# Kernel optimization log

Measured on AMD Instinct MI355X. Metric: run time of the kernel, lower is better.

## Reference

```python
import jax, jax.numpy as jnp
import numpy as np

EPS = 1e-5  # BatchNorm eps

def gcn_conv(x, src, dst, deg, dinv, W, b):
    # PyG GCNConv: out = D^{-1/2}(A+I)D^{-1/2} X W + b
    N = x.shape[0]
    xw = x @ W                               # [N, F_out]
    norm = dinv[src] * dinv[dst]             # [E]
    agg = jax.ops.segment_sum(xw[src] * norm[:, None], dst, num_segments=N)
    agg = agg + xw * (1.0 / deg)[:, None]    # self-loop term: deg^-1/2 * deg^-1/2
    return agg + b

def bn(x, g, b, m, v):
    # inference-mode BatchNorm1d over features
    return (x - m) * jax.lax.rsqrt(v + EPS) * g + b

def setup_inputs() -> dict:
    key = jax.random.key(0)
    N, E, F_in, C = 100000, 1600000, 128, 16
    dims = [F_in, 64, 128, 64, 32, C]
    ks = jax.random.split(key, 64)
    inp = {}
    inp["x"] = jax.random.normal(ks[0], (N, F_in), dtype=jnp.float32)
    inp["edge_index"] = jax.random.randint(ks[1], (2, E), 0, N, dtype=jnp.int32)
    ki = 2
    for l in range(5):
        fi, fo = dims[l], dims[l + 1]
        scale = 1.0 / np.sqrt(fi)
        inp[f"w{l+1}"] = jax.random.normal(ks[ki], (fi, fo), dtype=jnp.float32) * scale; ki += 1
        inp[f"b{l+1}"] = jnp.zeros((fo,), dtype=jnp.float32)
    for l in range(4):  # BN params for layers 1..4
        fo = dims[l + 1]
        inp[f"g{l+1}"] = jnp.ones((fo,), dtype=jnp.float32)
        inp[f"be{l+1}"] = jnp.zeros((fo,), dtype=jnp.float32)
        inp[f"m{l+1}"] = jax.random.normal(ks[ki], (fo,), dtype=jnp.float32) * 0.1; ki += 1
        inp[f"v{l+1}"] = jax.random.uniform(ks[ki], (fo,), dtype=jnp.float32, minval=0.5, maxval=1.5); ki += 1
    return inp

def reference(x, edge_index,
              w1, b1, w2, b2, w3, b3, w4, b4, w5, b5,
              g1, be1, m1, v1, g2, be2, m2, v2,
              g3, be3, m3, v3, g4, be4, m4, v4):
    N = x.shape[0]
    src, dst = edge_index[0], edge_index[1]
    deg = jax.ops.segment_sum(jnp.ones(src.shape[0], x.dtype), dst, num_segments=N) + 1.0
    dinv = jax.lax.rsqrt(deg)
    h = jax.nn.relu(bn(gcn_conv(x, src, dst, deg, dinv, w1, b1), g1, be1, m1, v1))
    h = jax.nn.relu(bn(gcn_conv(h, src, dst, deg, dinv, w2, b2), g2, be2, m2, v2))
    h = jax.nn.relu(bn(gcn_conv(h, src, dst, deg, dinv, w3, b3), g3, be3, m3, v3))
    h = jax.nn.relu(bn(gcn_conv(h, src, dst, deg, dinv, w4, b4), g4, be4, m4, v4))
    return gcn_conv(h, src, dst, deg, dinv, w5, b5)
```

## Files before the change

kernel.cpp:

```cpp
#include <hip/hip_runtime.h>
#include <hip/hip_fp16.h>

#define BEPS 1e-5f
static constexpr int TPB = 256;
static constexpr int G_SC = 512;
static constexpr int BK_SHIFT = 8;
static constexpr int BK_NODES = 256;
static constexpr int KMAX = 512;
static constexpr int BK_SLACK = 2048;

union F4H8 { float4 f4; __half2 h2[4]; };

typedef _Float16 half8 __attribute__((ext_vector_type(8)));
typedef float floatx4 __attribute__((ext_vector_type(4)));


__global__ __launch_bounds__(TPB) void k_zero_int(int* __restrict__ p, int n) {
  int i = blockIdx.x * TPB + threadIdx.x;
  if (i < n) p[i] = 0;
}

__global__ __launch_bounds__(TPB) void k_hist(const int* __restrict__ dst,
                                              int* __restrict__ histG,
                                              int* __restrict__ btot,
                                              int E, int K, int chunk) {
  __shared__ int lh[KMAX];
  int g = blockIdx.x, t = threadIdx.x;
  for (int i = t; i < KMAX; i += TPB) lh[i] = 0;
  __syncthreads();
  int e0 = g * chunk, e1 = min(E, e0 + chunk);
  for (int e = e0 + t; e < e1; e += TPB) atomicAdd(&lh[dst[e] >> BK_SHIFT], 1);
  __syncthreads();
  for (int i = t; i < K; i += TPB) {
    histG[i * G_SC + g] = lh[i];
    atomicAdd(&btot[i], lh[i]);
  }
}

__global__ __launch_bounds__(KMAX) void k_bbase(const int* __restrict__ btot,
                                                int* __restrict__ bbase, int K) {
  __shared__ int sh[KMAX];
  int t = threadIdx.x;
  int v = (t < K) ? btot[t] : 0;
  sh[t] = v;
  __syncthreads();
  for (int s = 1; s < KMAX; s <<= 1) {
    int x = sh[t];
    int y = (t >= s) ? sh[t - s] : 0;
    __syncthreads();
    sh[t] = x + y;
    __syncthreads();
  }
  if (t < K) bbase[t] = sh[t] - v;
  if (t == 0) bbase[K] = sh[K - 1];
}

__global__ __launch_bounds__(G_SC) void k_offs(const int* __restrict__ histG,
                                               const int* __restrict__ bbase,
                                               int* __restrict__ offs) {
  __shared__ int sh[G_SC];
  int b = blockIdx.x, t = threadIdx.x;
  int v = histG[b * G_SC + t];
  sh[t] = v;
  __syncthreads();
  for (int s = 1; s < G_SC; s <<= 1) {
    int x = sh[t];
    int y = (t >= s) ? sh[t - s] : 0;
    __syncthreads();
    sh[t] = x + y;
    __syncthreads();
  }
  offs[b * G_SC + t] = bbase[b] + sh[t] - v;
}

__global__ __launch_bounds__(TPB) void k_scatter(const int* __restrict__ src,
                                                 const int* __restrict__ dst,
                                                 const int* __restrict__ offs,
                                                 unsigned int* __restrict__ pairs,
                                                 int E, int K, int chunk) {
  __shared__ int cur[KMAX];
  int g = blockIdx.x, t = threadIdx.x;
  for (int i = t; i < K; i += TPB) cur[i] = offs[i * G_SC + g];
  __syncthreads();
  int e0 = g * chunk, e1 = min(E, e0 + chunk);
  for (int e = e0 + t; e < e1; e += TPB) {
    int d = dst[e];
    int b = d >> BK_SHIFT;
    int pos = atomicAdd(&cur[b], 1);
    pairs[pos] = (unsigned int)src[e] | ((unsigned int)(d & (BK_NODES - 1)) << 20);
  }
}

__global__ __launch_bounds__(TPB) void k_bucket_sort(const unsigned int* __restrict__ pairs,
                                                     const int* __restrict__ bbase,
                                                     int* __restrict__ rowptr,
                                                     int* __restrict__ rowend,
                                                     int* __restrict__ colidx,
                                                     float* __restrict__ dinv,
                                                     int N, int E) {
  __shared__ int cur[BK_NODES];
  __shared__ int sh[BK_NODES];
  int b = blockIdx.x, t = threadIdx.x;
  int base = bbase[b], end = bbase[b + 1];
  int n0 = b << BK_SHIFT;
  int nNodes = min(BK_NODES, N - n0);
  cur[t] = 0;
  __syncthreads();
  for (int e = base + t; e < end; e += TPB) atomicAdd(&cur[pairs[e] >> 20], 1);
  __syncthreads();
  int v = cur[t];
  int pd = (v + 7) & ~7;
  sh[t] = pd;
  __syncthreads();
  for (int s = 1; s < TPB; s <<= 1) {
    int x = sh[t];
    int y = (t >= s) ? sh[t - s] : 0;
    __syncthreads();
    sh[t] = x + y;
    __syncthreads();
  }
  int Bb = (base + b * BK_SLACK + 7) & ~7;
  int start = Bb + (sh[t] - pd);
  if (t < nNodes) {
    rowptr[n0 + t] = start;
    rowend[n0 + t] = start + pd;
    dinv[n0 + t] = rsqrtf((float)(v + 1));
    for (int i = start + v; i < start + pd; ++i) colidx[i] = N;
  }
  __syncthreads();
  cur[t] = start;
  __syncthreads();
  for (int e = base + t; e < end; e += TPB) {
    unsigned int p = pairs[e];
    int pos = atomicAdd(&cur[p >> 20], 1);
    colidx[pos] = (int)(p & 0xFFFFFu);
  }
}

__device__ inline void packone(const float* __restrict__ W, _Float16* __restrict__ Wp,
                               int i, int FO) {
  int j = i & 7, lane = (i >> 3) & 63, tile = i >> 9;
  int nct = FO >> 4, ct = tile % nct, kch = tile / nct;
  int k = kch * 32 + ((lane >> 4) << 3) + j;
  int n = (ct << 4) + (lane & 15);
  Wp[i] = (_Float16)W[k * FO + n];
}

__global__ __launch_bounds__(TPB) void k_packAll(const float* w1, _Float16* p1,
                                                 const float* w2, _Float16* p2,
                                                 const float* w3, _Float16* p3,
                                                 const float* w4, _Float16* p4,
                                                 const float* w5, _Float16* p5,
                                                 __half* bufA, int N) {
  int i = blockIdx.x * TPB + threadIdx.x;
  if (i < 8192) packone(w1, p1, i, 64);
  else if (i < 16384) packone(w2, p2, i - 8192, 128);
  else if (i < 24576) packone(w3, p3, i - 16384, 64);
  else if (i < 26624) packone(w4, p4, i - 24576, 32);
  else if (i < 27136) packone(w5, p5, i - 26624, 16);
  else if (i < 27144) {
    float4 z = {0.f, 0.f, 0.f, 0.f};
    reinterpret_cast<float4*>(bufA + (size_t)64 * N)[i - 27136] = z;
  }
}

template <int FI, int FO, int EPI, bool F32IN>
__global__ __launch_bounds__(TPB) void k_mgemm(const void* __restrict__ hin,
                                               const _Float16* __restrict__ Wp,
                                               const float* __restrict__ dinv,
                                               const float* __restrict__ bias,
                                               const float* __restrict__ g,
                                               const float* __restrict__ be,
                                               const float* __restrict__ m,
                                               const float* __restrict__ v,
                                               __half* __restrict__ out, int N) {
  constexpr int NCT = FO / 16;
  constexpr int NKC = FI / 32;
  __shared__ float4 Wsh[NKC * NCT * 64];
  for (int i = threadIdx.x; i < NKC * NCT * 64; i += TPB)
    Wsh[i] = reinterpret_cast<const float4*>(Wp)[i];
  __syncthreads();

  int lane = threadIdx.x & 63;
  int wv = threadIdx.x >> 6;
  int quad = lane >> 4;
  int rowBase = blockIdx.x * 64 + wv * 16;
  int rA = min(rowBase + (lane & 15), N - 1);

  floatx4 acc[NCT];
#pragma unroll
  for (int ct = 0; ct < NCT; ++ct) acc[ct] = (floatx4){0.f, 0.f, 0.f, 0.f};

#pragma unroll
  for (int kch = 0; kch < NKC; ++kch) {
    half8 a;
    if constexpr (F32IN) {
      const float4* xp = reinterpret_cast<const float4*>(hin);
      size_t idx = ((size_t)rA * FI + kch * 32 + quad * 8) >> 2;
      float4 fa = xp[idx], fb = xp[idx + 1];
      a[0] = (_Float16)fa.x; a[1] = (_Float16)fa.y; a[2] = (_Float16)fa.z; a[3] = (_Float16)fa.w;
      a[4] = (_Float16)fb.x; a[5] = (_Float16)fb.y; a[6] = (_Float16)fb.z; a[7] = (_Float16)fb.w;
    } else {
      union { float4 f4; half8 h8; } ua;
      ua.f4 = reinterpret_cast<const float4*>(hin)[((size_t)rA * FI + kch * 32 + quad * 8) >> 3];
      a = ua.h8;
    }
#pragma unroll
    for (int ct = 0; ct < NCT; ++ct) {
      union { float4 f4; half8 h8; } ub;
      ub.f4 = Wsh[(kch * NCT + ct) * 64 + lane];
      acc[ct] = __builtin_amdgcn_mfma_f32_16x16x32_f16(a, ub.h8, acc[ct], 0, 0, 0);
    }
  }

  int r0 = rowBase + quad * 4;
  if (EPI == 0) {
    float dv[4];
#pragma unroll
    for (int reg = 0; reg < 4; ++reg) dv[reg] = (r0 + reg < N) ? dinv[r0 + reg] : 0.f;
#pragma unroll
    for (int ct = 0; ct < NCT; ++ct) {
      int col = ct * 16 + (lane & 15);
#pragma unroll
      for (int reg = 0; reg < 4; ++reg) {
        int r = r0 + reg;
        out[(size_t)r * FO + col] = __float2half(acc[ct][reg] * dv[reg]);
      }
    }
  } else {
#pragma unroll
    for (int ct = 0; ct < NCT; ++ct) {
      int col = ct * 16 + (lane & 15);
      float sc = g[col] * rsqrtf(v[col] + BEPS);
      float bb = bias[col] - m[col];
      float ee = be[col];
#pragma unroll
      for (int reg = 0; reg < 4; ++reg) {
        int r = r0 + reg;
        out[(size_t)r * FO + col] = __float2half(fmaxf((acc[ct][reg] + bb) * sc + ee, 0.f));
      }
    }
  }
}

__global__ __launch_bounds__(TPB) void k_mgemm23(const __half* __restrict__ hin,
                                                 const _Float16* __restrict__ W2p,
                                                 const _Float16* __restrict__ W3p,
                                                 const float* __restrict__ dinv,
                                                 const float* __restrict__ b2,
                                                 const float* __restrict__ g2,
                                                 const float* __restrict__ be2,
                                                 const float* __restrict__ m2,
                                                 const float* __restrict__ v2,
                                                 __half* __restrict__ out, int N) {
  __shared__ float4 W2s[2 * 8 * 64];
  __shared__ float4 W3s[4 * 4 * 64];
  __shared__ _Float16 tr[4 * 16 * 136];
  for (int i = threadIdx.x; i < 1024; i += TPB) W2s[i] = reinterpret_cast<const float4*>(W2p)[i];
  for (int i = threadIdx.x; i < 1024; i += TPB) W3s[i] = reinterpret_cast<const float4*>(W3p)[i];
  __syncthreads();

  int lane = threadIdx.x & 63;
  int wv = threadIdx.x >> 6;
  int quad = lane >> 4;
  int m = lane & 15;
  int rowBase = blockIdx.x * 64 + wv * 16;
  int rA = min(rowBase + m, N - 1);

  floatx4 acc1[8];
#pragma unroll
  for (int ct = 0; ct < 8; ++ct) acc1[ct] = (floatx4){0.f, 0.f, 0.f, 0.f};
#pragma unroll
  for (int kch = 0; kch < 2; ++kch) {
    union { float4 f4; half8 h8; } ua;
    ua.f4 = reinterpret_cast<const float4*>(hin)[((size_t)rA * 64 + kch * 32 + quad * 8) >> 3];
#pragma unroll
    for (int ct = 0; ct < 8; ++ct) {
      union { float4 f4; half8 h8; } ub;
      ub.f4 = W2s[(kch * 8 + ct) * 64 + lane];
      acc1[ct] = __builtin_amdgcn_mfma_f32_16x16x32_f16(ua.h8, ub.h8, acc1[ct], 0, 0, 0);
    }
  }
  _Float16* mytr = tr + wv * 16 * 136;
#pragma unroll
  for (int ct = 0; ct < 8; ++ct) {
    int col = ct * 16 + m;
    float sc = g2[col] * rsqrtf(v2[col] + BEPS);
    float bb = b2[col] - m2[col];
    float ee = be2[col];
#pragma unroll
    for (int reg = 0; reg < 4; ++reg) {
      int r = quad * 4 + reg;
      mytr[r * 136 + col] = (_Float16)fmaxf((acc1[ct][reg] + bb) * sc + ee, 0.f);
    }
  }
  floatx4 acc2[4];
#pragma unroll
  for (int ct = 0; ct < 4; ++ct) acc2[ct] = (floatx4){0.f, 0.f, 0.f, 0.f};
#pragma unroll
  for (int kch = 0; kch < 4; ++kch) {
    half8 a2 = *reinterpret_cast<const half8*>(&mytr[m * 136 + kch * 32 + quad * 8]);
#pragma unroll
    for (int ct = 0; ct < 4; ++ct) {
      union { float4 f4; half8 h8; } ub;
      ub.f4 = W3s[(kch * 4 + ct) * 64 + lane];
      acc2[ct] = __builtin_amdgcn_mfma_f32_16x16x32_f16(a2, ub.h8, acc2[ct], 0, 0, 0);
    }
  }
  int r0 = rowBase + quad * 4;
  float dv[4];
#pragma unroll
  for (int reg = 0; reg < 4; ++reg) dv[reg] = (r0 + reg < N) ? dinv[r0 + reg] : 0.f;
#pragma unroll
  for (int ct = 0; ct < 4; ++ct) {
    int col = ct * 16 + m;
#pragma unroll
    for (int reg = 0; reg < 4; ++reg) {
      int r = r0 + reg;
      out[(size_t)r * 64 + col] = __float2half(acc2[ct][reg] * dv[reg]);
    }
  }
}

template <int F, int MODE, typename TO>
__global__ __launch_bounds__(TPB) void k_agg(const __half* __restrict__ in,
                                             const int* __restrict__ rowptr,
                                             const int* __restrict__ rowend,
                                             const int* __restrict__ colidx,
                                             const float* __restrict__ dinv,
                                             const float* __restrict__ bias,
                                             const float* __restrict__ g,
                                             const float* __restrict__ be,
                                             const float* __restrict__ m,
                                             const float* __restrict__ v,
                                             TO* __restrict__ out, int N) {
  constexpr int V = F / 8;
  constexpr int NPB = TPB / V;
  int node = blockIdx.x * NPB + (int)(threadIdx.x / V);
  int lane = threadIdx.x % V;
  if (node >= N) return;
  const float4* in16 = reinterpret_cast<const float4*>(in);
  const size_t rs = F / 8;
  float acc[8];
  {
    F4H8 u;
    u.f4 = in16[(size_t)node * rs + lane];
#pragma unroll
    for (int i = 0; i < 4; ++i) {
      float2 t2 = __half22float2(u.h2[i]);
      acc[2 * i] = t2.x;
      acc[2 * i + 1] = t2.y;
    }
  }
  int e0 = rowptr[node], e1 = rowend[node];
  int e = e0;
  for (; e + 16 <= e1; e += 16) {
    int4 c0 = *reinterpret_cast<const int4*>(colidx + e);
    int4 c1 = *reinterpret_cast<const int4*>(colidx + e + 4);
    int4 c2 = *reinterpret_cast<const int4*>(colidx + e + 8);
    int4 c3 = *reinterpret_cast<const int4*>(colidx + e + 12);
    F4H8 u[16];
    u[0].f4  = in16[(size_t)c0.x * rs + lane];
    u[1].f4  = in16[(size_t)c0.y * rs + lane];
    u[2].f4  = in16[(size_t)c0.z * rs + lane];
    u[3].f4  = in16[(size_t)c0.w * rs + lane];
    u[4].f4  = in16[(size_t)c1.x * rs + lane];
    u[5].f4  = in16[(size_t)c1.y * rs + lane];
    u[6].f4  = in16[(size_t)c1.z * rs + lane];
    u[7].f4  = in16[(size_t)c1.w * rs + lane];
    u[8].f4  = in16[(size_t)c2.x * rs + lane];
    u[9].f4  = in16[(size_t)c2.y * rs + lane];
    u[10].f4 = in16[(size_t)c2.z * rs + lane];
    u[11].f4 = in16[(size_t)c2.w * rs + lane];
    u[12].f4 = in16[(size_t)c3.x * rs + lane];
    u[13].f4 = in16[(size_t)c3.y * rs + lane];
    u[14].f4 = in16[(size_t)c3.z * rs + lane];
    u[15].f4 = in16[(size_t)c3.w * rs + lane];
#pragma unroll
    for (int q = 0; q < 16; ++q) {
#pragma unroll
      for (int i = 0; i < 4; ++i) {
        float2 t2 = __half22float2(u[q].h2[i]);
        acc[2 * i] += t2.x;
        acc[2 * i + 1] += t2.y;
      }
    }
  }
  if (e < e1) {
    int4 c0 = *reinterpret_cast<const int4*>(colidx + e);
    int4 c1 = *reinterpret_cast<const int4*>(colidx + e + 4);
    F4H8 u[8];
    u[0].f4 = in16[(size_t)c0.x * rs + lane];
    u[1].f4 = in16[(size_t)c0.y * rs + lane];
    u[2].f4 = in16[(size_t)c0.z * rs + lane];
    u[3].f4 = in16[(size_t)c0.w * rs + lane];
    u[4].f4 = in16[(size_t)c1.x * rs + lane];
    u[5].f4 = in16[(size_t)c1.y * rs + lane];
    u[6].f4 = in16[(size_t)c1.z * rs + lane];
    u[7].f4 = in16[(size_t)c1.w * rs + lane];
#pragma unroll
    for (int q = 0; q < 8; ++q) {
#pragma unroll
      for (int i = 0; i < 4; ++i) {
        float2 t2 = __half22float2(u[q].h2[i]);
        acc[2 * i] += t2.x;
        acc[2 * i + 1] += t2.y;
      }
    }
  }
  float dv = dinv[node];
#pragma unroll
  for (int i = 0; i < 8; ++i) acc[i] *= dv;
  if (MODE == 0) {
    float4 ba = reinterpret_cast<const float4*>(bias)[lane * 2];
    float4 bb = reinterpret_cast<const float4*>(bias)[lane * 2 + 1];
    acc[0] += ba.x; acc[1] += ba.y; acc[2] += ba.z; acc[3] += ba.w;
    acc[4] += bb.x; acc[5] += bb.y; acc[6] += bb.z; acc[7] += bb.w;
  } else if (MODE == 1 || MODE == 2) {
    const float4* B = reinterpret_cast<const float4*>(bias);
    const float4* G = reinterpret_cast<const float4*>(g);
    const float4* Be = reinterpret_cast<const float4*>(be);
    const float4* M = reinterpret_cast<const float4*>(m);
    const float4* Vv = reinterpret_cast<const float4*>(v);
#pragma unroll
    for (int h = 0; h < 2; ++h) {
      float4 b4 = B[lane * 2 + h], g4 = G[lane * 2 + h], e4 = Be[lane * 2 + h];
      float4 m4 = M[lane * 2 + h], v4 = Vv[lane * 2 + h];
      float* a = acc + 4 * h;
      a[0] = fmaxf((a[0] + b4.x - m4.x) * (g4.x * rsqrtf(v4.x + BEPS)) + e4.x, 0.f);
      a[1] = fmaxf((a[1] + b4.y - m4.y) * (g4.y * rsqrtf(v4.y + BEPS)) + e4.y, 0.f);
      a[2] = fmaxf((a[2] + b4.z - m4.z) * (g4.z * rsqrtf(v4.z + BEPS)) + e4.z, 0.f);
      a[3] = fmaxf((a[3] + b4.w - m4.w) * (g4.w * rsqrtf(v4.w + BEPS)) + e4.w, 0.f);
    }
    if (MODE == 2) {
#pragma unroll
      for (int i = 0; i < 8; ++i) acc[i] *= dv;
    }
  }
  if constexpr (sizeof(TO) == 2) {
    F4H8 u;
#pragma unroll
    for (int i = 0; i < 4; ++i) u.h2[i] = __floats2half2_rn(acc[2 * i], acc[2 * i + 1]);
    reinterpret_cast<float4*>(out)[(size_t)node * rs + lane] = u.f4;
  } else {
    float4 o0 = {acc[0], acc[1], acc[2], acc[3]};
    float4 o1 = {acc[4], acc[5], acc[6], acc[7]};
    float4* op = reinterpret_cast<float4*>((float*)out + (size_t)node * F + lane * 8);
    op[0] = o0;
    op[1] = o1;
  }
}


extern "C" void kernel_launch(void* const* d_in, const int* in_sizes, int n_in,
                              void* d_out, int out_size, void* d_ws, size_t ws_size,
                              hipStream_t stream) {
  const float* x = (const float*)d_in[0];
  const int* ei = (const int*)d_in[1];
  const int N = in_sizes[0] / 128;
  const int E = in_sizes[1] / 2;
  const int* src = ei;
  const int* dst = ei + E;

  const float* w1 = (const float*)d_in[2];  const float* b1 = (const float*)d_in[3];
  const float* w2 = (const float*)d_in[4];  const float* b2 = (const float*)d_in[5];
  const float* w3 = (const float*)d_in[6];  const float* b3 = (const float*)d_in[7];
  const float* w4 = (const float*)d_in[8];  const float* b4 = (const float*)d_in[9];
  const float* w5 = (const float*)d_in[10]; const float* b5 = (const float*)d_in[11];
  const float* g1 = (const float*)d_in[12]; const float* be1 = (const float*)d_in[13];
  const float* m1 = (const float*)d_in[14]; const float* v1 = (const float*)d_in[15];
  const float* g2 = (const float*)d_in[16]; const float* be2 = (const float*)d_in[17];
  const float* m2 = (const float*)d_in[18]; const float* v2 = (const float*)d_in[19];
  const float* g3 = (const float*)d_in[20]; const float* be3 = (const float*)d_in[21];
  const float* m3 = (const float*)d_in[22]; const float* v3 = (const float*)d_in[23];
  const float* g4 = (const float*)d_in[24]; const float* be4 = (const float*)d_in[25];
  const float* m4 = (const float*)d_in[26]; const float* v4 = (const float*)d_in[27];
  float* out = (float*)d_out;

  char* ws = (char*)d_ws;
  size_t off = 0;
  auto alloc = [&](size_t bytes) -> void* {
    void* p = ws + off;
    off += (bytes + 255) & ~(size_t)255;
    return p;
  };
  const int K = (N + BK_NODES - 1) >> BK_SHIFT;
  float*        dinv   = (float*)alloc((size_t)N * 4);
  int*          rowptr = (int*)alloc((size_t)N * 4);
  int*          rowend = (int*)alloc((size_t)N * 4);
  int*          colidx = (int*)alloc(((size_t)E + (size_t)(K + 1) * BK_SLACK) * 4);
  unsigned int* pairs  = (unsigned int*)alloc((size_t)E * 4);
  int*          histG  = (int*)alloc((size_t)KMAX * G_SC * 4);
  int*          offs   = (int*)alloc((size_t)KMAX * G_SC * 4);
  int*          btot   = (int*)alloc(KMAX * 4);
  int*          bbase  = (int*)alloc((KMAX + 1) * 4);
  _Float16*     wp1    = (_Float16*)alloc(128 * 64 * 2);
  _Float16*     wp2    = (_Float16*)alloc(64 * 128 * 2);
  _Float16*     wp3    = (_Float16*)alloc(128 * 64 * 2);
  _Float16*     wp4    = (_Float16*)alloc(64 * 32 * 2);
  _Float16*     wp5    = (_Float16*)alloc(32 * 16 * 2);
  __half*       bufA   = (__half*)alloc((size_t)(N + 64) * 128 * 2);
  __half*       bufB   = (__half*)alloc((size_t)(N + 64) * 128 * 2);
  (void)ws_size; (void)n_in; (void)out_size;

  const int chunk = (E + G_SC - 1) / G_SC;

  k_zero_int<<<2, TPB, 0, stream>>>(btot, KMAX);
  k_hist<<<G_SC, TPB, 0, stream>>>(dst, histG, btot, E, K, chunk);
  k_bbase<<<1, KMAX, 0, stream>>>(btot, bbase, K);
  k_offs<<<K, G_SC, 0, stream>>>(histG, bbase, offs);
  k_scatter<<<G_SC, TPB, 0, stream>>>(src, dst, offs, pairs, E, K, chunk);
  k_bucket_sort<<<K, TPB, 0, stream>>>(pairs, bbase, rowptr, rowend, colidx, dinv, N, E);

  k_packAll<<<(27144 + TPB - 1) / TPB, TPB, 0, stream>>>(w1, wp1, w2, wp2, w3, wp3, w4, wp4, w5, wp5, bufA, N);

  int gRow = (N + 63) / 64;
  k_mgemm<128, 64, 0, true><<<gRow, TPB, 0, stream>>>(x, wp1, dinv, nullptr, nullptr, nullptr, nullptr, nullptr, bufB, N);
  k_agg<64, 2, __half><<<(N + 31) / 32, TPB, 0, stream>>>(bufB, rowptr, rowend, colidx, dinv, b1, g1, be1, m1, v1, bufA, N);
  k_agg<64, 3, __half><<<(N + 31) / 32, TPB, 0, stream>>>(bufA, rowptr, rowend, colidx, dinv, nullptr, nullptr, nullptr, nullptr, nullptr, bufB, N);
  k_mgemm23<<<gRow, TPB, 0, stream>>>(bufB, wp2, wp3, dinv, b2, g2, be2, m2, v2, bufA, N);
  k_agg<64, 1, __half><<<(N + 31) / 32, TPB, 0, stream>>>(bufA, rowptr, rowend, colidx, dinv, b3, g3, be3, m3, v3, bufB, N);
  k_mgemm<64, 32, 0, false><<<gRow, TPB, 0, stream>>>(bufB, wp4, dinv, nullptr, nullptr, nullptr, nullptr, nullptr, bufA, N);
  k_agg<32, 1, __half><<<(N + 63) / 64, TPB, 0, stream>>>(bufA, rowptr, rowend, colidx, dinv, b4, g4, be4, m4, v4, bufB, N);
  k_mgemm<32, 16, 0, false><<<gRow, TPB, 0, stream>>>(bufB, wp5, dinv, nullptr, nullptr, nullptr, nullptr, nullptr, bufA, N);
  k_agg<16, 0, float><<<(N + 127) / 128, TPB, 0, stream>>>(bufA, rowptr, rowend, colidx, dinv, b5, nullptr, nullptr, nullptr, nullptr, out, N);
}
```

Before: 360.4 us.

## Fuse neighbor aggregation into following GEMM kernels for layers two through five

Replaces the separate aggregate-then-GEMM kernel pairs for the later layers with fused kernels that gather neighbor rows, apply normalization and BN/ReLU in registers, and feed the result straight into MFMA. This removes intermediate feature-buffer writes and reads and several launches. The histogram and scatter preprocessing kernels also switch to int4 vectorized edge loads, with the chunk size rounded up to a multiple of four. The fused gather assigns one node per 16-lane group with 4-way unrolling, so it may have less memory-level parallelism than the dedicated aggregation kernel. It also relies on column lists being padded to multiples of four.

```diff
diff --git a/kernel.cpp b/kernel.cpp
--- a/kernel.cpp
+++ b/kernel.cpp
@@ -29,7 +29,17 @@
   for (int i = t; i < KMAX; i += TPB) lh[i] = 0;
   __syncthreads();
   int e0 = g * chunk, e1 = min(E, e0 + chunk);
-  for (int e = e0 + t; e < e1; e += TPB) atomicAdd(&lh[dst[e] >> BK_SHIFT], 1);
+  for (int e = e0 + t * 4; e < e1; e += TPB * 4) {
+    if (e + 4 <= e1) {
+      int4 d4 = *reinterpret_cast<const int4*>(dst + e);
+      atomicAdd(&lh[d4.x >> BK_SHIFT], 1);
+      atomicAdd(&lh[d4.y >> BK_SHIFT], 1);
+      atomicAdd(&lh[d4.z >> BK_SHIFT], 1);
+      atomicAdd(&lh[d4.w >> BK_SHIFT], 1);
+    } else {
+      for (int q = e; q < e1; ++q) atomicAdd(&lh[dst[q] >> BK_SHIFT], 1);
+    }
+  }
   __syncthreads();
   for (int i = t; i < K; i += TPB) {
     histG[i * G_SC + g] = lh[i];
@@ -83,11 +93,25 @@
   for (int i = t; i < K; i += TPB) cur[i] = offs[i * G_SC + g];
   __syncthreads();
   int e0 = g * chunk, e1 = min(E, e0 + chunk);
-  for (int e = e0 + t; e < e1; e += TPB) {
-    int d = dst[e];
-    int b = d >> BK_SHIFT;
-    int pos = atomicAdd(&cur[b], 1);
-    pairs[pos] = (unsigned int)src[e] | ((unsigned int)(d & (BK_NODES - 1)) << 20);
+  for (int e = e0 + t * 4; e < e1; e += TPB * 4) {
+    if (e + 4 <= e1) {
+      int4 d4 = *reinterpret_cast<const int4*>(dst + e);
+      int4 s4 = *reinterpret_cast<const int4*>(src + e);
+      int p0 = atomicAdd(&cur[d4.x >> BK_SHIFT], 1);
+      pairs[p0] = (unsigned int)s4.x | ((unsigned int)(d4.x & (BK_NODES - 1)) << 20);
+      int p1 = atomicAdd(&cur[d4.y >> BK_SHIFT], 1);
+      pairs[p1] = (unsigned int)s4.y | ((unsigned int)(d4.y & (BK_NODES - 1)) << 20);
+      int p2 = atomicAdd(&cur[d4.z >> BK_SHIFT], 1);
+      pairs[p2] = (unsigned int)s4.z | ((unsigned int)(d4.z & (BK_NODES - 1)) << 20);
+      int p3 = atomicAdd(&cur[d4.w >> BK_SHIFT], 1);
+      pairs[p3] = (unsigned int)s4.w | ((unsigned int)(d4.w & (BK_NODES - 1)) << 20);
+    } else {
+      for (int q = e; q < e1; ++q) {
+        int d = dst[q];
+        int pos = atomicAdd(&cur[d >> BK_SHIFT], 1);
+        pairs[pos] = (unsigned int)src[q] | ((unsigned int)(d & (BK_NODES - 1)) << 20);
+      }
+    }
   }
 }
 
@@ -214,45 +238,98 @@
   }
 
   int r0 = rowBase + quad * 4;
-  if (EPI == 0) {
-    float dv[4];
-#pragma unroll
-    for (int reg = 0; reg < 4; ++reg) dv[reg] = (r0 + reg < N) ? dinv[r0 + reg] : 0.f;
-#pragma unroll
-    for (int ct = 0; ct < NCT; ++ct) {
-      int col = ct * 16 + (lane & 15);
-#pragma unroll
-      for (int reg = 0; reg < 4; ++reg) {
-        int r = r0 + reg;
-        out[(size_t)r * FO + col] = __float2half(acc[ct][reg] * dv[reg]);
+  float dv[4];
+#pragma unroll
+  for (int reg = 0; reg < 4; ++reg) dv[reg] = (r0 + reg < N) ? dinv[r0 + reg] : 0.f;
+#pragma unroll
+  for (int ct = 0; ct < NCT; ++ct) {
+    int col = ct * 16 + (lane & 15);
+#pragma unroll
+    for (int reg = 0; reg < 4; ++reg) {
+      int r = r0 + reg;
+      out[(size_t)r * FO + col] = __float2half(acc[ct][reg] * dv[reg]);
+    }
+  }
+  (void)bias; (void)g; (void)be; (void)m; (void)v;
+}
+
+template <int DO_BN>
+__device__ inline void agg_gather64(const float4* __restrict__ in16,
+                                    const int* __restrict__ rowptr,
+                                    const int* __restrict__ rowend,
+                                    const int* __restrict__ colidx,
+                                    const float* __restrict__ dinv,
+                                    const float* __restrict__ b_,
+                                    const float* __restrict__ g_,
+                                    const float* __restrict__ be_,
+                                    const float* __restrict__ m_,
+                                    const float* __restrict__ v_,
+                                    int node, int quad, int N, half8 afr[2]) {
+  bool valid = node < N;
+  int rd = valid ? node : N;
+  int e0 = valid ? rowptr[node] : 0;
+  int e1 = valid ? rowend[node] : 0;
+  float acc[2][8];
+#pragma unroll
+  for (int kch = 0; kch < 2; ++kch) {
+    F4H8 u;
+    u.f4 = in16[(size_t)rd * 8 + kch * 4 + quad];
+#pragma unroll
+    for (int i = 0; i < 4; ++i) {
+      float2 t2 = __half22float2(u.h2[i]);
+      acc[kch][2 * i] = t2.x;
+      acc[kch][2 * i + 1] = t2.y;
+    }
+  }
+  for (int e = e0; e < e1; e += 4) {
+    int4 c = *reinterpret_cast<const int4*>(colidx + e);
+#pragma unroll
+    for (int kch = 0; kch < 2; ++kch) {
+      int g = kch * 4 + quad;
+      F4H8 u0, u1, u2, u3;
+      u0.f4 = in16[(size_t)c.x * 8 + g];
+      u1.f4 = in16[(size_t)c.y * 8 + g];
+      u2.f4 = in16[(size_t)c.z * 8 + g];
+      u3.f4 = in16[(size_t)c.w * 8 + g];
+#pragma unroll
+      for (int i = 0; i < 4; ++i) {
+        float2 a = __half22float2(u0.h2[i]), b = __half22float2(u1.h2[i]);
+        float2 cc = __half22float2(u2.h2[i]), d = __half22float2(u3.h2[i]);
+        acc[kch][2 * i] += (a.x + b.x) + (cc.x + d.x);
+        acc[kch][2 * i + 1] += (a.y + b.y) + (cc.y + d.y);
       }
     }
-  } else {
-#pragma unroll
-    for (int ct = 0; ct < NCT; ++ct) {
-      int col = ct * 16 + (lane & 15);
-      float sc = g[col] * rsqrtf(v[col] + BEPS);
-      float bb = bias[col] - m[col];
-      float ee = be[col];
-#pragma unroll
-      for (int reg = 0; reg < 4; ++reg) {
-        int r = r0 + reg;
-        out[(size_t)r * FO + col] = __float2half(fmaxf((acc[ct][reg] + bb) * sc + ee, 0.f));
+  }
+  float dv = valid ? dinv[node] : 0.f;
+#pragma unroll
+  for (int kch = 0; kch < 2; ++kch) {
+    int f0 = kch * 32 + quad * 8;
+#pragma unroll
+    for (int j = 0; j < 8; ++j) {
+      float val = acc[kch][j] * dv;
+      if (DO_BN) {
+        int f = f0 + j;
+        float sc = g_[f] * rsqrtf(v_[f] + BEPS);
+        val = fmaxf((val + b_[f] - m_[f]) * sc + be_[f], 0.f);
       }
-    }
-  }
-}
-
-__global__ __launch_bounds__(TPB) void k_mgemm23(const __half* __restrict__ hin,
-                                                 const _Float16* __restrict__ W2p,
-                                                 const _Float16* __restrict__ W3p,
-                                                 const float* __restrict__ dinv,
-                                                 const float* __restrict__ b2,
-                                                 const float* __restrict__ g2,
-                                                 const float* __restrict__ be2,
-                                                 const float* __restrict__ m2,
-                                                 const float* __restrict__ v2,
-                                                 __half* __restrict__ out, int N) {
+      afr[kch][j] = (_Float16)val;
+    }
+  }
+}
+
+__global__ __launch_bounds__(TPB) void k_aggemm23(const __half* __restrict__ hin,
+                                                  const int* __restrict__ rowptr,
+                                                  const int* __restrict__ rowend,
+                                                  const int* __restrict__ colidx,
+                                                  const _Float16* __restrict__ W2p,
+                                                  const _Float16* __restrict__ W3p,
+                                                  const float* __restrict__ dinv,
+                                                  const float* __restrict__ b2,
+                                                  const float* __restrict__ g2,
+                                                  const float* __restrict__ be2,
+                                                  const float* __restrict__ m2,
+                                                  const float* __restrict__ v2,
+                                                  __half* __restrict__ out, int N) {
   __shared__ float4 W2s[2 * 8 * 64];
   __shared__ float4 W3s[4 * 4 * 64];
   __shared__ _Float16 tr[4 * 16 * 136];
@@ -265,20 +342,21 @@
   int quad = lane >> 4;
   int m = lane & 15;
   int rowBase = blockIdx.x * 64 + wv * 16;
-  int rA = min(rowBase + m, N - 1);
+
+  half8 afr[2];
+  agg_gather64<0>(reinterpret_cast<const float4*>(hin), rowptr, rowend, colidx, dinv,
+                  nullptr, nullptr, nullptr, nullptr, nullptr, rowBase + m, quad, N, afr);
 
   floatx4 acc1[8];
 #pragma unroll
   for (int ct = 0; ct < 8; ++ct) acc1[ct] = (floatx4){0.f, 0.f, 0.f, 0.f};
 #pragma unroll
   for (int kch = 0; kch < 2; ++kch) {
-    union { float4 f4; half8 h8; } ua;
-    ua.f4 = reinterpret_cast<const float4*>(hin)[((size_t)rA * 64 + kch * 32 + quad * 8) >> 3];
 #pragma unroll
     for (int ct = 0; ct < 8; ++ct) {
       union { float4 f4; half8 h8; } ub;
       ub.f4 = W2s[(kch * 8 + ct) * 64 + lane];
-      acc1[ct] = __builtin_amdgcn_mfma_f32_16x16x32_f16(ua.h8, ub.h8, acc1[ct], 0, 0, 0);
+      acc1[ct] = __builtin_amdgcn_mfma_f32_16x16x32_f16(afr[kch], ub.h8, acc1[ct], 0, 0, 0);
     }
   }
   _Float16* mytr = tr + wv * 16 * 136;
@@ -319,6 +397,138 @@
       int r = r0 + reg;
       out[(size_t)r * 64 + col] = __float2half(acc2[ct][reg] * dv[reg]);
     }
+  }
+}
+
+template <int FO>
+__global__ __launch_bounds__(TPB) void k_aggemm64(const __half* __restrict__ hin,
+                                                  const int* __restrict__ rowptr,
+                                                  const int* __restrict__ rowend,
+                                                  const int* __restrict__ colidx,
+                                                  const _Float16* __restrict__ Wp,
+                                                  const float* __restrict__ dinv,
+                                                  const float* __restrict__ b_,
+                                                  const float* __restrict__ g_,
+                                                  const float* __restrict__ be_,
+                                                  const float* __restrict__ m_,
+                                                  const float* __restrict__ v_,
+                                                  __half* __restrict__ out, int N) {
+  constexpr int NCT = FO / 16;
+  __shared__ float4 Wsh[2 * NCT * 64];
+  for (int i = threadIdx.x; i < 2 * NCT * 64; i += TPB)
+    Wsh[i] = reinterpret_cast<const float4*>(Wp)[i];
+  __syncthreads();
+
+  int lane = threadIdx.x & 63;
+  int wv = threadIdx.x >> 6;
+  int quad = lane >> 4;
+  int m = lane & 15;
+  int rowBase = blockIdx.x * 64 + wv * 16;
+
+  half8 afr[2];
+  agg_gather64<1>(reinterpret_cast<const float4*>(hin), rowptr, rowend, colidx, dinv,
+                  b_, g_, be_, m_, v_, rowBase + m, quad, N, afr);
+
+  floatx4 acc[NCT];
+#pragma unroll
+  for (int ct = 0; ct < NCT; ++ct) acc[ct] = (floatx4){0.f, 0.f, 0.f, 0.f};
+#pragma unroll
+  for (int kch = 0; kch < 2; ++kch) {
+#pragma unroll
+    for (int ct = 0; ct < NCT; ++ct) {
+      union { float4 f4; half8 h8; } ub;
+      ub.f4 = Wsh[(kch * NCT + ct) * 64 + lane];
+      acc[ct] = __builtin_amdgcn_mfma_f32_16x16x32_f16(afr[kch], ub.h8, acc[ct], 0, 0, 0);
+    }
+  }
+  int r0 = rowBase + quad * 4;
+  float dv[4];
+#pragma unroll
+  for (int reg = 0; reg < 4; ++reg) dv[reg] = (r0 + reg < N) ? dinv[r0 + reg] : 0.f;
+#pragma unroll
+  for (int ct = 0; ct < NCT; ++ct) {
+    int col = ct * 16 + m;
+#pragma unroll
+    for (int reg = 0; reg < 4; ++reg) {
+      int r = r0 + reg;
+      out[(size_t)r * FO + col] = __float2half(acc[ct][reg] * dv[reg]);
+    }
+  }
+}
+
+__global__ __launch_bounds__(TPB) void k_aggemm5(const __half* __restrict__ hin,
+                                                 const int* __restrict__ rowptr,
+                                                 const int* __restrict__ rowend,
+                                                 const int* __restrict__ colidx,
+                                                 const _Float16* __restrict__ Wp,
+                                                 const float* __restrict__ dinv,
+                                                 const float* __restrict__ b_,
+                                                 const float* __restrict__ g_,
+                                                 const float* __restrict__ be_,
+                                                 const float* __restrict__ m_,
+                                                 const float* __restrict__ v_,
+                                                 __half* __restrict__ out, int N) {
+  __shared__ float4 Wsh[64];
+  if (threadIdx.x < 64) Wsh[threadIdx.x] = reinterpret_cast<const float4*>(Wp)[threadIdx.x];
+  __syncthreads();
+
+  int lane = threadIdx.x & 63;
+  int wv = threadIdx.x >> 6;
+  int quad = lane >> 4;
+  int m = lane & 15;
+  int rowBase = blockIdx.x * 64 + wv * 16;
+  int node = rowBase + m;
+  bool valid = node < N;
+  int rd = valid ? node : N;
+  int e0 = valid ? rowptr[node] : 0;
+  int e1 = valid ? rowend[node] : 0;
+  const float4* in16 = reinterpret_cast<const float4*>(hin);
+
+  float acc[8];
+  {
+    F4H8 u;
+    u.f4 = in16[(size_t)rd * 4 + quad];
+#pragma unroll
+    for (int i = 0; i < 4; ++i) {
+      float2 t2 = __half22float2(u.h2[i]);
+      acc[2 * i] = t2.x;
+      acc[2 * i + 1] = t2.y;
+    }
+  }
+  for (int e = e0; e < e1; e += 4) {
+    int4 c = *reinterpret_cast<const int4*>(colidx + e);
+    F4H8 u0, u1, u2, u3;
+    u0.f4 = in16[(size_t)c.x * 4 + quad];
+    u1.f4 = in16[(size_t)c.y * 4 + quad];
+    u2.f4 = in16[(size_t)c.z * 4 + quad];
+    u3.f4 = in16[(size_t)c.w * 4 + quad];
+#pragma unroll
+    for (int i = 0; i < 4; ++i) {
+      float2 a = __half22float2(u0.h2[i]), b = __half22float2(u1.h2[i]);
+      float2 cc = __half22float2(u2.h2[i]), d = __half22float2(u3.h2[i]);
+      acc[2 * i] += (a.x + b.x) + (cc.x + d.x);
+      acc[2 * i + 1] += (a.y + b.y) + (cc.y + d.y);
+    }
+  }
+  float dvn = valid ? dinv[node] : 0.f;
+  half8 afr;
+#pragma unroll
+  for (int j = 0; j < 8; ++j) {
+    int f = quad * 8 + j;
+    float sc = g_[f] * rsqrtf(v_[f] + BEPS);
+    float val = fmaxf((acc[j] * dvn + b_[f] - m_[f]) * sc + be_[f], 0.f);
+    afr[j] = (_Float16)val;
+  }
+  floatx4 c0 = (floatx4){0.f, 0.f, 0.f, 0.f};
+  union { float4 f4; half8 h8; } ub;
+  ub.f4 = Wsh[lane];
+  c0 = __builtin_amdgcn_mfma_f32_16x16x32_f16(afr, ub.h8, c0, 0, 0, 0);
+  int r0 = rowBase + quad * 4;
+#pragma unroll
+  for (int reg = 0; reg < 4; ++reg) {
+    int r = r0 + reg;
+    float dv = (r < N) ? dinv[r] : 0.f;
+    out[(size_t)r * 16 + m] = __float2half(c0[reg] * dv);
   }
 }
 
@@ -354,39 +564,7 @@
   }
   int e0 = rowptr[node], e1 = rowend[node];
   int e = e0;
-  for (; e + 16 <= e1; e += 16) {
-    int4 c0 = *reinterpret_cast<const int4*>(colidx + e);
-    int4 c1 = *reinterpret_cast<const int4*>(colidx + e + 4);
-    int4 c2 = *reinterpret_cast<const int4*>(colidx + e + 8);
-    int4 c3 = *reinterpret_cast<const int4*>(colidx + e + 12);
-    F4H8 u[16];
-    u[0].f4  = in16[(size_t)c0.x * rs + lane];
-    u[1].f4  = in16[(size_t)c0.y * rs + lane];
-    u[2].f4  = in16[(size_t)c0.z * rs + lane];
-    u[3].f4  = in16[(size_t)c0.w * rs + lane];
-    u[4].f4  = in16[(size_t)c1.x * rs + lane];
-    u[5].f4  = in16[(size_t)c1.y * rs + lane];
-    u[6].f4  = in16[(size_t)c1.z * rs + lane];
-    u[7].f4  = in16[(size_t)c1.w * rs + lane];
-    u[8].f4  = in16[(size_t)c2.x * rs + lane];
-    u[9].f4  = in16[(size_t)c2.y * rs + lane];
-    u[10].f4 = in16[(size_t)c2.z * rs + lane];
-    u[11].f4 = in16[(size_t)c2.w * rs + lane];
-    u[12].f4 = in16[(size_t)c3.x * rs + lane];
-    u[13].f4 = in16[(size_t)c3.y * rs + lane];
-    u[14].f4 = in16[(size_t)c3.z * rs + lane];
-    u[15].f4 = in16[(size_t)c3.w * rs + lane];
-#pragma unroll
-    for (int q = 0; q < 16; ++q) {
-#pragma unroll
-      for (int i = 0; i < 4; ++i) {
-        float2 t2 = __half22float2(u[q].h2[i]);
-        acc[2 * i] += t2.x;
-        acc[2 * i + 1] += t2.y;
-      }
-    }
-  }
-  if (e < e1) {
+  for (; e + 8 <= e1; e += 8) {
     int4 c0 = *reinterpret_cast<const int4*>(colidx + e);
     int4 c1 = *reinterpret_cast<const int4*>(colidx + e + 4);
     F4H8 u[8];
@@ -503,7 +681,7 @@
   __half*       bufB   = (__half*)alloc((size_t)(N + 64) * 128 * 2);
   (void)ws_size; (void)n_in; (void)out_size;
 
-  const int chunk = (E + G_SC - 1) / G_SC;
+  const int chunk = (((E + G_SC - 1) / G_SC) + 3) & ~3;
 
   k_zero_int<<<2, TPB, 0, stream>>>(btot, KMAX);
   k_hist<<<G_SC, TPB, 0, stream>>>(dst, histG, btot, E, K, chunk);
@@ -517,11 +695,8 @@
   int gRow = (N + 63) / 64;
   k_mgemm<128, 64, 0, true><<<gRow, TPB, 0, stream>>>(x, wp1, dinv, nullptr, nullptr, nullptr, nullptr, nullptr, bufB, N);
   k_agg<64, 2, __half><<<(N + 31) / 32, TPB, 0, stream>>>(bufB, rowptr, rowend, colidx, dinv, b1, g1, be1, m1, v1, bufA, N);
-  k_agg<64, 3, __half><<<(N + 31) / 32, TPB, 0, stream>>>(bufA, rowptr, rowend, colidx, dinv, nullptr, nullptr, nullptr, nullptr, nullptr, bufB, N);
-  k_mgemm23<<<gRow, TPB, 0, stream>>>(bufB, wp2, wp3, dinv, b2, g2, be2, m2, v2, bufA, N);
-  k_agg<64, 1, __half><<<(N + 31) / 32, TPB, 0, stream>>>(bufA, rowptr, rowend, colidx, dinv, b3, g3, be3, m3, v3, bufB, N);
-  k_mgemm<64, 32, 0, false><<<gRow, TPB, 0, stream>>>(bufB, wp4, dinv, nullptr, nullptr, nullptr, nullptr, nullptr, bufA, N);
-  k_agg<32, 1, __half><<<(N + 63) / 64, TPB, 0, stream>>>(bufA, rowptr, rowend, colidx, dinv, b4, g4, be4, m4, v4, bufB, N);
-  k_mgemm<32, 16, 0, false><<<gRow, TPB, 0, stream>>>(bufB, wp5, dinv, nullptr, nullptr, nullptr, nullptr, nullptr, bufA, N);
-  k_agg<16, 0, float><<<(N + 127) / 128, TPB, 0, stream>>>(bufA, rowptr, rowend, colidx, dinv, b5, nullptr, nullptr, nullptr, nullptr, out, N);
-}
+  k_aggemm23<<<gRow, TPB, 0, stream>>>(bufA, rowptr, rowend, colidx, wp2, wp3, dinv, b2, g2, be2, m2, v2, bufB, N);
+  k_aggemm64<32><<<gRow, TPB, 0, stream>>>(bufB, rowptr, rowend, colidx, wp4, dinv, b3, g3, be3, m3, v3, bufA, N);
+  k_aggemm5<<<gRow, TPB, 0, stream>>>(bufA, rowptr, rowend, colidx, wp5, dinv, b4, g4, be4, m4, v4, bufB, N);
+  k_agg<16, 0, float><<<(N + 127) / 128, TPB, 0, stream>>>(bufB, rowptr, rowend, colidx, dinv, b5, nullptr, nullptr, nullptr, nullptr, out, N);
+}
```

Result: no change. 364.3 us (+1.1%).
